# Performance work log

Measured on AMD Instinct MI355X. Metric: run time of the kernel, lower is better.

Reference implementation:

```python
import jax, jax.numpy as jnp
import numpy as np

B, C, IMG, P, D, L, NH, DFF = 8, 2, 256, 16, 1024, 8, 16, 4096
HP = IMG // P          # 16 patches per side
N = HP * HP            # 256 patch tokens
S = N + 1              # + cls token
HD = D // NH           # 64 head dim


def _ln(x, w, b, eps=1e-5):
    mu = x.mean(-1, keepdims=True)
    var = ((x - mu) ** 2).mean(-1, keepdims=True)
    return (x - mu) * jax.lax.rsqrt(var + eps) * w + b


def _decay_mask():
    # RetNetRelPos2d(D, NH, initial_value=1, heads_range=NH): per-head log-decay
    decay = jnp.log(1.0 - 2.0 ** (-1.0 - NH * jnp.arange(NH, dtype=jnp.float32) / NH))
    idx = jnp.arange(HP)
    gy, gx = jnp.meshgrid(idx, idx, indexing='ij')
    grid = jnp.stack([gy.ravel(), gx.ravel()], -1)                 # [N,2]
    dist = jnp.abs(grid[:, None] - grid[None, :]).sum(-1)          # [N,N] Manhattan
    mask = decay[:, None, None] * dist.astype(jnp.float32)        # [NH,N,N]
    return jnp.pad(mask, ((0, 0), (1, 0), (1, 0)))                 # cls: zero decay


def setup_inputs() -> dict:
    key = jax.random.key(0)
    ks = iter(jax.random.split(key, 16))
    g = lambda shape: jax.random.normal(next(ks), shape, jnp.float32) * 0.02
    return dict(
        imgs=jax.random.normal(next(ks), (B, C, IMG, IMG), jnp.float32),
        patch_w=g((C, P, P, D)), patch_b=jnp.zeros((D,), jnp.float32),
        cls_tok=g((1, 1, D)),
        ln1_w=jnp.ones((L, D), jnp.float32), ln1_b=jnp.zeros((L, D), jnp.float32),
        wq=g((L, D, D)), wk=g((L, D, D)), wv=g((L, D, D)),
        bq=jnp.zeros((L, D), jnp.float32), bk=jnp.zeros((L, D), jnp.float32), bv=jnp.zeros((L, D), jnp.float32),
        wo=g((L, D, D)), bo=jnp.zeros((L, D), jnp.float32),
        ln2_w=jnp.ones((L, D), jnp.float32), ln2_b=jnp.zeros((L, D), jnp.float32),
        w1=g((L, D, DFF)), b1=jnp.zeros((L, DFF), jnp.float32),
        w2=g((L, DFF, D)), b2=jnp.zeros((L, D), jnp.float32),
        normf_w=jnp.ones((D,), jnp.float32), normf_b=jnp.zeros((D,), jnp.float32),
        enpred_w=g((D, P * P * 2)), enpred_b=jnp.zeros((P * P * 2,), jnp.float32),
    )


def reference(imgs, patch_w, patch_b, cls_tok, ln1_w, ln1_b, wq, wk, wv, bq, bk, bv,
              wo, bo, ln2_w, ln2_b, w1, b1, w2, b2, normf_w, normf_b, enpred_w, enpred_b):
    b = imgs.shape[0]
    # PatchEmbed: conv with stride==kernel == patch extraction + linear
    xp = imgs.reshape(b, C, HP, P, HP, P)
    x = jnp.einsum('nchpwq,cpqd->nhwd', xp, patch_w).reshape(b, N, D) + patch_b
    residual = x
    x = jnp.concatenate([jnp.broadcast_to(cls_tok, (b, 1, D)), x], axis=1)  # [b,S,D]
    mask = _decay_mask()  # [NH,S,S]
    scale = HD ** -0.5
    for i in range(L):  # RMT blocks: pre-LN MaSA (softmax(qk*scale + decay)) + pre-LN GELU MLP
        h = _ln(x, ln1_w[i], ln1_b[i])
        q = (h @ wq[i] + bq[i]).reshape(b, S, NH, HD)
        k = (h @ wk[i] + bk[i]).reshape(b, S, NH, HD)
        v = (h @ wv[i] + bv[i]).reshape(b, S, NH, HD)
        logits = jnp.einsum('bqhd,bkhd->bhqk', q, k) * scale + mask
        attn = jax.nn.softmax(logits, axis=-1)
        o = jnp.einsum('bhqk,bkhd->bqhd', attn, v).reshape(b, S, D)
        x = x + o @ wo[i] + bo[i]
        h = _ln(x, ln2_w[i], ln2_b[i])
        x = x + jax.nn.gelu(h @ w1[i] + b1[i], approximate=False) @ w2[i] + b2[i]
    x = _ln(x, normf_w, normf_b)
    # PGSA on patch tokens as [b,D,HP,HP]
    t = x[:, 1:, :].transpose(0, 2, 1).reshape(b, D, HP, HP)
    n = HP * HP - 1
    mu = t.mean(axis=(2, 3), keepdims=True)
    xm2 = (t - mu) ** 2
    y = xm2 / (4.0 * (xm2.sum(axis=(2, 3), keepdims=True) / n + 1e-4)) + 0.5
    t = t * jax.nn.sigmoid(y)
    tokens = t.reshape(b, D, N).transpose(0, 2, 1) + residual
    pred = tokens @ enpred_w + enpred_b  # [b,N,P*P*2]
    # unpatchify -> [b,2,IMG,IMG]
    u = pred.reshape(b, HP, HP, P, P, 2)
    return jnp.einsum('nhwpqc->nchpwq', u).reshape(b, 2, IMG, IMG)
```

## Files before the change

### kernel.cpp

```cpp
#include <hip/hip_runtime.h>
#include <cstdint>
#include <cstddef>

#define BB    8
#define CCH   2
#define IMGD  256
#define PDIM  16
#define DD    1024
#define LLAY  8
#define NHEAD 16
#define DFFD  4096
#define NTOK  256
#define SD    257
#define HDD   64
#define MTOK  (BB*SD)
#define MPAT  (BB*NTOK)
#define MPAD  2176
#define KPAD  288

typedef unsigned short u16;
typedef __bf16 bf16x8 __attribute__((ext_vector_type(8)));
typedef float  f32x4  __attribute__((ext_vector_type(4)));

__device__ __forceinline__ u16 f2bf(float f) {
    uint32_t u = __float_as_uint(f);
    u += 0x7FFF + ((u >> 16) & 1);
    return (u16)(u >> 16);
}
__device__ __forceinline__ int imin(int a, int b) { return a < b ? a : b; }

#define GLB(p)  ((const __attribute__((address_space(1))) void*)(uintptr_t)(p))
#define LDSP(p) ((__attribute__((address_space(3))) void*)(uint32_t)(uintptr_t)(p))

__device__ __forceinline__ void tp64(const float* __restrict__ W,
                                     u16* __restrict__ WT, int K, int N,
                                     int k0, int n0, float (*t)[65])
{
    const int c = threadIdx.x & 63, r4 = threadIdx.x >> 6;
    #pragma unroll
    for (int i = 0; i < 16; ++i) {
        const int r = i * 4 + r4;
        t[r][c] = W[(size_t)(k0 + r) * N + n0 + c];
    }
    __syncthreads();
    #pragma unroll
    for (int i = 0; i < 16; ++i) {
        const int r = i * 4 + r4;
        WT[(size_t)(n0 + r) * K + k0 + c] = f2bf(t[c][r]);
    }
}

__device__ __forceinline__ void tp_dispatch(
    int t, const float* wqN, const float* wkN, const float* wvN,
    const float* woN, const float* w1N, const float* w2N,
    u16* WTqkvN, u16* WTwoN, u16* WTw1N, u16* WTw2N, float (*tb)[65])
{
    if (t < 768) {
        const int which = t >> 8, local = t & 255;
        const float* W = which == 0 ? wqN : which == 1 ? wkN : wvN;
        tp64(W, WTqkvN + (size_t)which * 1024 * DD, DD, DD,
             (local >> 4) * 64, (local & 15) * 64, tb);
    } else if (t < 1024) {
        const int local = t - 768;
        tp64(woN, WTwoN, DD, DD, (local >> 4) * 64, (local & 15) * 64, tb);
    } else if (t < 2048) {
        const int local = t - 1024;
        tp64(w1N, WTw1N, DD, DFFD, (local >> 6) * 64, (local & 63) * 64, tb);
    } else {
        const int local = t - 2048;
        tp64(w2N, WTw2N, DFFD, DD, (local >> 4) * 64, (local & 15) * 64, tb);
    }
}

__global__ __launch_bounds__(256) void mlp1_tp(
    const u16* __restrict__ A, const u16* __restrict__ BT,
    const float* __restrict__ bias, u16* __restrict__ Cout, int M,
    const float* __restrict__ wqN, const float* __restrict__ wkN,
    const float* __restrict__ wvN, const float* __restrict__ woN,
    const float* __restrict__ w1N, const float* __restrict__ w2N,
    u16* __restrict__ WTqkvN, u16* __restrict__ WTwoN,
    u16* __restrict__ WTw1N, u16* __restrict__ WTw2N)
{
    __shared__ float smem[64 * 65];
    if (blockIdx.y >= 17) {
        const int t = (blockIdx.y - 17) * 32 + blockIdx.x;
        tp_dispatch(t, wqN, wkN, wvN, woN, w1N, w2N,
                    WTqkvN, WTwoN, WTw1N, WTw2N, (float(*)[65])smem);
        return;
    }
    u16* lds = (u16*)smem;
    const int N = DFFD, K = DD;
    const int tid = threadIdx.x, wid = tid >> 6, lane = tid & 63;
    const int m0 = blockIdx.y * 128, n0 = blockIdx.x * 128;
    const int wm = (wid >> 1) * 64, wn = (wid & 1) * 64;
    const int srow = lane >> 2, scol = (lane & 3) * 8;
    const int l15 = lane & 15, loct = lane >> 4;

    f32x4 acc[4][4] = {};
    const size_t arow = (size_t)(m0 + wid * 16 + srow) * K + scol;
    const size_t brow = (size_t)(n0 + wid * 16 + srow) * K + scol;
    u16* ldsA = lds + wid * 512;
    u16* ldsB = lds + 4096 + wid * 512;

    for (int k0 = 0; k0 < K; k0 += 32) {
        __builtin_amdgcn_global_load_lds(GLB(A  + arow + k0),                 LDSP(ldsA),        16, 0, 0);
        __builtin_amdgcn_global_load_lds(GLB(A  + arow + (size_t)64*K + k0),  LDSP(ldsA + 2048), 16, 0, 0);
        __builtin_amdgcn_global_load_lds(GLB(BT + brow + k0),                 LDSP(ldsB),        16, 0, 0);
        __builtin_amdgcn_global_load_lds(GLB(BT + brow + (size_t)64*K + k0),  LDSP(ldsB + 2048), 16, 0, 0);
        __syncthreads();
        bf16x8 af[4], bfr[4];
        #pragma unroll
        for (int i = 0; i < 4; ++i)
            af[i] = *(const bf16x8*)(lds + (wm + i * 16 + l15) * 32 + loct * 8);
        #pragma unroll
        for (int j = 0; j < 4; ++j)
            bfr[j] = *(const bf16x8*)(lds + 4096 + (wn + j * 16 + l15) * 32 + loct * 8);
        #pragma unroll
        for (int i = 0; i < 4; ++i)
            #pragma unroll
            for (int j = 0; j < 4; ++j)
                acc[i][j] = __builtin_amdgcn_mfma_f32_16x16x32_bf16(af[i], bfr[j], acc[i][j], 0, 0, 0);
        __syncthreads();
    }

    #pragma unroll
    for (int j = 0; j < 4; ++j) {
        const int col = n0 + wn + j * 16 + l15;
        const float bv = bias[col];
        #pragma unroll
        for (int i = 0; i < 4; ++i) {
            const int rbase = m0 + wm + i * 16 + loct * 4;
            #pragma unroll
            for (int r = 0; r < 4; ++r) {
                const int row = rbase + r;
                if (row < M) {
                    float v = acc[i][j][r] + bv;
                    v = 0.5f * v * (1.f + erff(v * 0.70710678118654752f));
                    Cout[(size_t)row * N + col] = f2bf(v);
                }
            }
        }
    }
}

__global__ __launch_bounds__(256) void patch_tp(
    const u16* __restrict__ A, const u16* __restrict__ BT,
    const float* __restrict__ bias, float* __restrict__ Cout,
    const float* __restrict__ wq0, const float* __restrict__ wk0,
    const float* __restrict__ wv0, const float* __restrict__ wo0,
    const float* __restrict__ w10, const float* __restrict__ w20,
    u16* __restrict__ WTqkv0, u16* __restrict__ WTwo0,
    u16* __restrict__ WTw10, u16* __restrict__ WTw20)
{
    __shared__ float smem[64 * 65];
    if (blockIdx.y >= 32) {
        const int t = (blockIdx.y - 32) * 16 + blockIdx.x;
        tp_dispatch(t, wq0, wk0, wv0, wo0, w10, w20,
                    WTqkv0, WTwo0, WTw10, WTw20, (float(*)[65])smem);
        return;
    }
    u16* lds = (u16*)smem;
    const int N = DD, K = 512;
    const int tid = threadIdx.x, wid = tid >> 6, lane = tid & 63;
    const int m0 = blockIdx.y * 64, n0 = blockIdx.x * 64;
    const int wm = (wid >> 1) * 32, wn = (wid & 1) * 32;
    const int srow = lane >> 2, scol = (lane & 3) * 8;
    const int l15 = lane & 15, loct = lane >> 4;

    f32x4 acc[2][2] = {};
    const size_t arow = (size_t)(m0 + wid * 16 + srow) * K + scol;
    const size_t brow = (size_t)(n0 + wid * 16 + srow) * K + scol;
    u16* ldsA = lds + wid * 512;
    u16* ldsB = lds + 4096 + wid * 512;

    for (int k0 = 0; k0 < K; k0 += 64) {
        __builtin_amdgcn_global_load_lds(GLB(A  + arow + k0),      LDSP(ldsA),        16, 0, 0);
        __builtin_amdgcn_global_load_lds(GLB(A  + arow + k0 + 32), LDSP(ldsA + 2048), 16, 0, 0);
        __builtin_amdgcn_global_load_lds(GLB(BT + brow + k0),      LDSP(ldsB),        16, 0, 0);
        __builtin_amdgcn_global_load_lds(GLB(BT + brow + k0 + 32), LDSP(ldsB + 2048), 16, 0, 0);
        __syncthreads();
        #pragma unroll
        for (int t = 0; t < 2; ++t) {
            bf16x8 af[2], bfr[2];
            #pragma unroll
            for (int i = 0; i < 2; ++i)
                af[i] = *(const bf16x8*)(lds + t * 2048 + (wm + i * 16 + l15) * 32 + loct * 8);
            #pragma unroll
            for (int j = 0; j < 2; ++j)
                bfr[j] = *(const bf16x8*)(lds + 4096 + t * 2048 + (wn + j * 16 + l15) * 32 + loct * 8);
            #pragma unroll
            for (int i = 0; i < 2; ++i)
                #pragma unroll
                for (int j = 0; j < 2; ++j)
                    acc[i][j] = __builtin_amdgcn_mfma_f32_16x16x32_bf16(af[i], bfr[j], acc[i][j], 0, 0, 0);
        }
        __syncthreads();
    }

    #pragma unroll
    for (int j = 0; j < 2; ++j) {
        const int col = n0 + wn + j * 16 + l15;
        const float bv = bias[col];
        #pragma unroll
        for (int i = 0; i < 2; ++i) {
            const int rbase = m0 + wm + i * 16 + loct * 4;
            #pragma unroll
            for (int r = 0; r < 4; ++r) {
                const int row = rbase + r;
                Cout[(size_t)row * N + col] = acc[i][j][r] + bv;
            }
        }
    }
}

__global__ __launch_bounds__(256) void gemm_qkv(
    const u16* __restrict__ A, const u16* __restrict__ BT,
    const float* __restrict__ bq, const float* __restrict__ bk,
    const float* __restrict__ bvp,
    u16* __restrict__ QKb, u16* __restrict__ VTg, int M, int K)
{
    __shared__ u16 lds[8192];
    const int tid = threadIdx.x, wid = tid >> 6, lane = tid & 63;
    const int m0 = blockIdx.y * 128, n0 = blockIdx.x * 128;
    const int wm = (wid >> 1) * 64, wn = (wid & 1) * 64;
    const int srow = lane >> 2, scol = (lane & 3) * 8;
    const int l15 = lane & 15, loct = lane >> 4;

    f32x4 acc[4][4] = {};
    const size_t arow = (size_t)(m0 + wid * 16 + srow) * K + scol;
    const size_t brow = (size_t)(n0 + wid * 16 + srow) * K + scol;
    u16* ldsA = lds + wid * 512;
    u16* ldsB = lds + 4096 + wid * 512;

    for (int k0 = 0; k0 < K; k0 += 32) {
        __builtin_amdgcn_global_load_lds(GLB(A  + arow + k0),                 LDSP(ldsA),        16, 0, 0);
        __builtin_amdgcn_global_load_lds(GLB(A  + arow + (size_t)64*K + k0),  LDSP(ldsA + 2048), 16, 0, 0);
        __builtin_amdgcn_global_load_lds(GLB(BT + brow + k0),                 LDSP(ldsB),        16, 0, 0);
        __builtin_amdgcn_global_load_lds(GLB(BT + brow + (size_t)64*K + k0),  LDSP(ldsB + 2048), 16, 0, 0);
        __syncthreads();
        bf16x8 af[4], bfr[4];
        #pragma unroll
        for (int i = 0; i < 4; ++i)
            af[i] = *(const bf16x8*)(lds + (wm + i * 16 + l15) * 32 + loct * 8);
        #pragma unroll
        for (int j = 0; j < 4; ++j)
            bfr[j] = *(const bf16x8*)(lds + 4096 + (wn + j * 16 + l15) * 32 + loct * 8);
        #pragma unroll
        for (int i = 0; i < 4; ++i)
            #pragma unroll
            for (int j = 0; j < 4; ++j)
                acc[i][j] = __builtin_amdgcn_mfma_f32_16x16x32_bf16(af[i], bfr[j], acc[i][j], 0, 0, 0);
        __syncthreads();
    }

    #pragma unroll
    for (int j = 0; j < 4; ++j) {
        const int col = n0 + wn + j * 16 + l15;
        const float bval = (col < 1024) ? bq[col]
                         : (col < 2048) ? bk[col - 1024]
                                        : bvp[col - 2048];
        #pragma unroll
        for (int i = 0; i < 4; ++i) {
            const int rbase = m0 + wm + i * 16 + loct * 4;
            #pragma unroll
            for (int r = 0; r < 4; ++r) {
                const int row = rbase + r;
                if (row < M) {
                    const float v = acc[i][j][r] + bval;
                    if (col < 2048) {
                        QKb[(size_t)row * 2048 + col] = f2bf(v);
                    } else {
                        const int b = row / SD;
                        const int key = row - b * SD;
                        VTg[((size_t)b * 1024 + (col - 2048)) * KPAD + key] = f2bf(v);
                    }
                }
            }
        }
    }
}

template<int ACT, int OBF>
__global__ __launch_bounds__(256) void gemm64(
    const u16* __restrict__ A, const u16* __restrict__ BT,
    const float* __restrict__ bias, const float* __restrict__ Cin,
    void* __restrict__ Cout, int M, int N, int K)
{
    __shared__ u16 lds[8192];
    const int tid = threadIdx.x, wid = tid >> 6, lane = tid & 63;
    const int m0 = blockIdx.y * 64, n0 = blockIdx.x * 64;
    const int wm = (wid >> 1) * 32, wn = (wid & 1) * 32;
    const int srow = lane >> 2, scol = (lane & 3) * 8;
    const int l15 = lane & 15, loct = lane >> 4;

    f32x4 acc[2][2] = {};
    const size_t arow = (size_t)(m0 + wid * 16 + srow) * K + scol;
    const size_t brow = (size_t)(n0 + wid * 16 + srow) * K + scol;
    u16* ldsA = lds + wid * 512;
    u16* ldsB = lds + 4096 + wid * 512;

    for (int k0 = 0; k0 < K; k0 += 64) {
        __builtin_amdgcn_global_load_lds(GLB(A  + arow + k0),      LDSP(ldsA),        16, 0, 0);
        __builtin_amdgcn_global_load_lds(GLB(A  + arow + k0 + 32), LDSP(ldsA + 2048), 16, 0, 0);
        __builtin_amdgcn_global_load_lds(GLB(BT + brow + k0),      LDSP(ldsB),        16, 0, 0);
        __builtin_amdgcn_global_load_lds(GLB(BT + brow + k0 + 32), LDSP(ldsB + 2048), 16, 0, 0);
        __syncthreads();
        #pragma unroll
        for (int t = 0; t < 2; ++t) {
            bf16x8 af[2], bfr[2];
            #pragma unroll
            for (int i = 0; i < 2; ++i)
                af[i] = *(const bf16x8*)(lds + t * 2048 + (wm + i * 16 + l15) * 32 + loct * 8);
            #pragma unroll
            for (int j = 0; j < 2; ++j)
                bfr[j] = *(const bf16x8*)(lds + 4096 + t * 2048 + (wn + j * 16 + l15) * 32 + loct * 8);
            #pragma unroll
            for (int i = 0; i < 2; ++i)
                #pragma unroll
                for (int j = 0; j < 2; ++j)
                    acc[i][j] = __builtin_amdgcn_mfma_f32_16x16x32_bf16(af[i], bfr[j], acc[i][j], 0, 0, 0);
        }
        __syncthreads();
    }

    #pragma unroll
    for (int j = 0; j < 2; ++j) {
        const int col = n0 + wn + j * 16 + l15;
        const float bv = bias[col];
        #pragma unroll
        for (int i = 0; i < 2; ++i) {
            const int rbase = m0 + wm + i * 16 + loct * 4;
            #pragma unroll
            for (int r = 0; r < 4; ++r) {
                const int row = rbase + r;
                if (row < M) {
                    float v = acc[i][j][r] + bv;
                    if (ACT) v = 0.5f * v * (1.f + erff(v * 0.70710678118654752f));
                    if (Cin) v += Cin[(size_t)row * N + col];
                    if (OBF) ((u16*)Cout)[(size_t)row * N + col] = f2bf(v);
                    else     ((float*)Cout)[(size_t)row * N + col] = v;
                }
            }
        }
    }
}

__global__ __launch_bounds__(256) void attn_fused(
    const u16* __restrict__ QKb, const u16* __restrict__ VTg,
    u16* __restrict__ O)
{
    __shared__ u16 P[4][16][296];
    const int tid = threadIdx.x, wid = tid >> 6, lane = tid & 63;
    const int l15 = lane & 15, loct = lane >> 4;
    const int bh = blockIdx.x, b = bh >> 4, h = bh & 15;
    const int q0 = blockIdx.y * 64 + wid * 16;

    const size_t qkbase = (size_t)b * SD * 2048 + h * 64;
    const u16* qp = QKb + qkbase + (size_t)imin(q0 + l15, SD - 1) * 2048;
    const bf16x8 qf0 = *(const bf16x8*)(qp + loct * 8);
    const bf16x8 qf1 = *(const bf16x8*)(qp + 32 + loct * 8);

    f32x4 s[17];
    #pragma unroll
    for (int nt = 0; nt < 17; ++nt) {
        const u16* kp = QKb + qkbase + (size_t)imin(nt * 16 + l15, SD - 1) * 2048 + 1024;
        const bf16x8 kf0 = *(const bf16x8*)(kp + loct * 8);
        const bf16x8 kf1 = *(const bf16x8*)(kp + 32 + loct * 8);
        f32x4 a = {};
        a = __builtin_amdgcn_mfma_f32_16x16x32_bf16(qf0, kf0, a, 0, 0, 0);
        a = __builtin_amdgcn_mfma_f32_16x16x32_bf16(qf1, kf1, a, 0, 0, 0);
        s[nt] = a;
    }

    const float dec = logf(1.f - exp2f(-1.f - (float)h));
    const int qb = q0 + loct * 4;
    float rmax[4] = {-3.4e38f, -3.4e38f, -3.4e38f, -3.4e38f};
    #pragma unroll
    for (int nt = 0; nt < 17; ++nt) {
        const int key = nt * 16 + l15;
        #pragma unroll
        for (int r = 0; r < 4; ++r) {
            float v;
            if (key >= SD) {
                v = -1e30f;
            } else {
                v = s[nt][r] * 0.125f;
                const int q = qb + r;
                if (q > 0 && key > 0) {
                    const int nq = q - 1, nk = key - 1;
                    const int dist = abs((nq >> 4) - (nk >> 4)) + abs((nq & 15) - (nk & 15));
                    v += dec * (float)dist;
                }
            }
            s[nt][r] = v;
            rmax[r] = fmaxf(rmax[r], v);
        }
    }
    #pragma unroll
    for (int r = 0; r < 4; ++r) {
        #pragma unroll
        for (int m = 1; m < 16; m <<= 1) rmax[r] = fmaxf(rmax[r], __shfl_xor(rmax[r], m));
    }
    float rsum[4] = {0.f, 0.f, 0.f, 0.f};
    #pragma unroll
    for (int nt = 0; nt < 17; ++nt)
        #pragma unroll
        for (int r = 0; r < 4; ++r) {
            const float e = __expf(s[nt][r] - rmax[r]);
            s[nt][r] = e;
            rsum[r] += e;
        }
    #pragma unroll
    for (int r = 0; r < 4; ++r) {
        #pragma unroll
        for (int m = 1; m < 16; m <<= 1) rsum[r] += __shfl_xor(rsum[r], m);
        rsum[r] = 1.f / rsum[r];
    }
    #pragma unroll
    for (int nt = 0; nt < 17; ++nt)
        #pragma unroll
        for (int r = 0; r < 4; ++r)
            P[wid][loct * 4 + r][nt * 16 + l15] = f2bf(s[nt][r] * rsum[r]);
    {
        const int rr = lane >> 2, cc = (lane & 3) * 4;
        #pragma unroll
        for (int i = 0; i < 4; ++i) P[wid][rr][272 + cc + i] = 0;
    }

    f32x4 o[4] = {};
    const u16* vrow = VTg + ((size_t)b * 1024 + h * 64) * KPAD;
    #pragma unroll
    for (int ks = 0; ks < 9; ++ks) {
        const bf16x8 pf = *(const bf16x8*)&P[wid][l15][ks * 32 + loct * 8];
        #pragma unroll
        for (int j = 0; j < 4; ++j) {
            const bf16x8 vf = *(const bf16x8*)(vrow + (size_t)(j * 16 + l15) * KPAD + ks * 32 + loct * 8);
            o[j] = __builtin_amdgcn_mfma_f32_16x16x32_bf16(pf, vf, o[j], 0, 0, 0);
        }
    }
    #pragma unroll
    for (int j = 0; j < 4; ++j)
        #pragma unroll
        for (int r = 0; r < 4; ++r) {
            const int q = qb + r;
            if (q < SD) O[((size_t)(b * SD + q)) * DD + h * 64 + j * 16 + l15] = f2bf(o[j][r]);
        }
}

__global__ __launch_bounds__(256) void transpose_bf16_b(
    const float* __restrict__ W, u16* __restrict__ WT, int K, int N,
    size_t sstrideZ, size_t dstrideZ)
{
    __shared__ float t[64][65];
    tp64(W + (size_t)blockIdx.z * sstrideZ, WT + (size_t)blockIdx.z * dstrideZ,
         K, N, blockIdx.y * 64, blockIdx.x * 64, t);
}

__global__ __launch_bounds__(256) void im2col_k(const float* __restrict__ imgs,
                                                u16* __restrict__ Ao)
{
    const int idx = blockIdx.x * 256 + threadIdx.x;
    const int k = idx & 511, m = idx >> 9;
    const int b = m >> 8, n = m & 255;
    const int hp = n >> 4, wp = n & 15;
    const int c = k >> 8, p = (k >> 4) & 15, q = k & 15;
    Ao[idx] = f2bf(imgs[(((size_t)b * CCH + c) * IMGD + hp * PDIM + p) * IMGD + wp * PDIM + q]);
}

__global__ __launch_bounds__(256) void build_x_k(const float* __restrict__ RES,
                                                 const float* __restrict__ cls,
                                                 float* __restrict__ X)
{
    const int idx = blockIdx.x * 256 + threadIdx.x;
    const int d = idx & 1023;
    const int r = idx >> 10;
    const int b = r / SD;
    const int s = r - b * SD;
    X[idx] = (s == 0) ? cls[d] : RES[((size_t)(b * NTOK + s - 1)) * DD + d];
}

template<int OBF>
__global__ __launch_bounds__(256) void ln_rows(const float* __restrict__ X,
                                               const float* __restrict__ w,
                                               const float* __restrict__ bsrc,
                                               void* __restrict__ Y)
{
    const int wid = threadIdx.x >> 6, lane = threadIdx.x & 63;
    const int row = blockIdx.x * 4 + wid;
    const float* xr = X + (size_t)row * DD;
    float4 v[4];
    float s = 0.f, s2 = 0.f;
    #pragma unroll
    for (int i = 0; i < 4; ++i) {
        v[i] = *(const float4*)(xr + (i * 64 + lane) * 4);
        s  += v[i].x + v[i].y + v[i].z + v[i].w;
        s2 += v[i].x * v[i].x + v[i].y * v[i].y + v[i].z * v[i].z + v[i].w * v[i].w;
    }
    #pragma unroll
    for (int off = 1; off < 64; off <<= 1) {
        s  += __shfl_xor(s, off);
        s2 += __shfl_xor(s2, off);
    }
    const float mu  = s * (1.f / 1024.f);
    const float var = fmaf(-mu, mu, s2 * (1.f / 1024.f));
    const float ri  = rsqrtf(var + 1e-5f);
    #pragma unroll
    for (int i = 0; i < 4; ++i) {
        const float4 wv = *(const float4*)(w + (i * 64 + lane) * 4);
        const float4 bv = *(const float4*)(bsrc + (i * 64 + lane) * 4);
        float4 o;
        o.x = (v[i].x - mu) * ri * wv.x + bv.x;
        o.y = (v[i].y - mu) * ri * wv.y + bv.y;
        o.z = (v[i].z - mu) * ri * wv.z + bv.z;
        o.w = (v[i].w - mu) * ri * wv.w + bv.w;
        if (OBF) {
            ushort4 o4 = make_ushort4(f2bf(o.x), f2bf(o.y), f2bf(o.z), f2bf(o.w));
            *(ushort4*)((u16*)Y + (size_t)row * DD + (i * 64 + lane) * 4) = o4;
        } else {
            *(float4*)((float*)Y + (size_t)row * DD + (i * 64 + lane) * 4) = o;
        }
    }
}

__global__ __launch_bounds__(256) void pgsa_k(const float* __restrict__ Xf,
                                              const float* __restrict__ RES,
                                              u16* __restrict__ TOK)
{
    const int bd = blockIdx.x;
    const int b = bd >> 10, dch = bd & 1023;
    const int n = threadIdx.x;
    const float t = Xf[((size_t)(b * SD + 1 + n)) * DD + dch];
    __shared__ float red[4];
    float s = t;
    #pragma unroll
    for (int off = 1; off < 64; off <<= 1) s += __shfl_xor(s, off);
    if ((n & 63) == 0) red[n >> 6] = s;
    __syncthreads();
    const float mu = (red[0] + red[1] + red[2] + red[3]) * (1.f / 256.f);
    const float xm = t - mu;
    const float xm2 = xm * xm;
    __syncthreads();
    float s2 = xm2;
    #pragma unroll
    for (int off = 1; off < 64; off <<= 1) s2 += __shfl_xor(s2, off);
    if ((n & 63) == 0) red[n >> 6] = s2;
    __syncthreads();
    const float tot2 = red[0] + red[1] + red[2] + red[3];
    const float y = xm2 / (4.f * (tot2 * (1.f / 255.f) + 1e-4f)) + 0.5f;
    const float sig = 1.f / (1.f + expf(-y));
    const size_t ri = ((size_t)b * NTOK + n) * DD + dch;
    TOK[ri] = f2bf(fmaf(t, sig, RES[ri]));
}

__global__ __launch_bounds__(256) void unpatch_k(const float* __restrict__ PRED,
                                                 float* __restrict__ out)
{
    const int idx = blockIdx.x * 256 + threadIdx.x;
    const int j = idx & 255, i = (idx >> 8) & 255;
    const int c = (idx >> 16) & 1, b = idx >> 17;
    const int hp = i >> 4, p = i & 15, wp = j >> 4, q = j & 15;
    out[idx] = PRED[((size_t)b * NTOK + hp * 16 + wp) * 512 + (p * 16 + q) * 2 + c];
}

extern "C" void kernel_launch(void* const* d_in, const int* in_sizes, int n_in,
                              void* d_out, int out_size, void* d_ws, size_t ws_size,
                              hipStream_t stream)
{
    const float* imgs     = (const float*)d_in[0];
    const float* patch_w  = (const float*)d_in[1];
    const float* patch_b  = (const float*)d_in[2];
    const float* cls_tok  = (const float*)d_in[3];
    const float* ln1_w    = (const float*)d_in[4];
    const float* ln1_b    = (const float*)d_in[5];
    const float* wq       = (const float*)d_in[6];
    const float* wk       = (const float*)d_in[7];
    const float* wv       = (const float*)d_in[8];
    const float* bq       = (const float*)d_in[9];
    const float* bk       = (const float*)d_in[10];
    const float* bv       = (const float*)d_in[11];
    const float* wo       = (const float*)d_in[12];
    const float* bo       = (const float*)d_in[13];
    const float* ln2_w    = (const float*)d_in[14];
    const float* ln2_b    = (const float*)d_in[15];
    const float* w1       = (const float*)d_in[16];
    const float* b1       = (const float*)d_in[17];
    const float* w2       = (const float*)d_in[18];
    const float* b2       = (const float*)d_in[19];
    const float* normf_w  = (const float*)d_in[20];
    const float* normf_b  = (const float*)d_in[21];
    const float* enpred_w = (const float*)d_in[22];
    const float* enpred_b = (const float*)d_in[23];
    float* out = (float*)d_out;

    char* w = (char*)d_ws;
    float* X     = (float*)w;            w += (size_t)MTOK * DD * 4;
    float* RES   = (float*)w;            w += (size_t)MPAT * DD * 4;
    u16*   QKb   = (u16*)w;              w += (size_t)MPAD * 2048 * 2;
    u16*   VTg   = (u16*)w;              w += (size_t)BB * 1024 * KPAD * 2;
    char*  UNION = w;                    w += (size_t)MPAD * DFFD * 2;
    u16*   Hb    = (u16*)w;              w += (size_t)MPAD * DD * 2;
    u16*   Ob    = (u16*)w;              w += (size_t)MPAD * DD * 2;
    u16*   WTqkv = (u16*)w;              w += (size_t)LLAY * 3072 * DD * 2;
    u16*   WTwo  = (u16*)w;              w += (size_t)LLAY * DD * DD * 2;
    u16*   WTw1  = (u16*)w;              w += (size_t)LLAY * DFFD * DD * 2;
    u16*   WTw2  = (u16*)w;              w += (size_t)LLAY * DD * DFFD * 2;
    u16*   WTpe  = (u16*)w;              w += (size_t)DD * 512 * 2;
    u16*   WTen  = (u16*)w;              w += (size_t)512 * DD * 2;

    u16*   IM2b  = (u16*)UNION;
    u16*   GELUb = (u16*)UNION;
    float* PRED  = (float*)UNION;
    float* Hf    = (float*)QKb;
    u16*   TOKb  = Hb;

    hipMemsetAsync(VTg, 0, (size_t)BB * 1024 * KPAD * 2, stream);

    hipLaunchKernelGGL(transpose_bf16_b, dim3(DD / 64, 512 / 64, 1), dim3(256), 0, stream,
                       patch_w, WTpe, 512, DD, (size_t)0, (size_t)0);
    hipLaunchKernelGGL(transpose_bf16_b, dim3(512 / 64, DD / 64, 1), dim3(256), 0, stream,
                       enpred_w, WTen, DD, 512, (size_t)0, (size_t)0);
    hipLaunchKernelGGL(im2col_k, dim3(4096), dim3(256), 0, stream, imgs, IM2b);

    hipLaunchKernelGGL(patch_tp, dim3(DD / 64, 32 + 192), dim3(256), 0, stream,
                       IM2b, WTpe, patch_b, RES,
                       wq, wk, wv, wo, w1, w2,
                       WTqkv, WTwo, WTw1, WTw2);
    hipLaunchKernelGGL(build_x_k, dim3(MTOK * DD / 256), dim3(256), 0, stream, RES, cls_tok, X);

    for (int i = 0; i < LLAY; ++i) {
        hipLaunchKernelGGL((ln_rows<1>), dim3(MTOK / 4), dim3(256), 0, stream,
                           X, ln1_w + i * DD, ln1_b + i * DD, (void*)Hb);
        hipLaunchKernelGGL(gemm_qkv, dim3(3072 / 128, 17), dim3(256), 0, stream,
                           Hb, WTqkv + (size_t)i * 3072 * DD,
                           bq + i * DD, bk + i * DD, bv + i * DD, QKb, VTg, MTOK, DD);
        hipLaunchKernelGGL(attn_fused, dim3(BB * NHEAD, 5), dim3(256), 0, stream,
                           QKb, VTg, Ob);
        hipLaunchKernelGGL((gemm64<0,0>), dim3(DD / 64, 33), dim3(256), 0, stream,
                           Ob, WTwo + (size_t)i * DD * DD, bo + i * DD, X, (void*)X, MTOK, DD, DD);
        hipLaunchKernelGGL((ln_rows<1>), dim3(MTOK / 4), dim3(256), 0, stream,
                           X, ln2_w + i * DD, ln2_b + i * DD, (void*)Hb);
        if (i < LLAY - 1) {
            const size_t n1 = (size_t)(i + 1);
            hipLaunchKernelGGL(mlp1_tp, dim3(DFFD / 128, 17 + 96), dim3(256), 0, stream,
                               Hb, WTw1 + (size_t)i * DFFD * DD, b1 + i * DFFD, GELUb, MTOK,
                               wq + n1 * DD * DD, wk + n1 * DD * DD, wv + n1 * DD * DD,
                               wo + n1 * DD * DD, w1 + n1 * DD * DFFD, w2 + n1 * DFFD * DD,
                               WTqkv + n1 * 3072 * DD, WTwo + n1 * DD * DD,
                               WTw1 + n1 * DFFD * DD, WTw2 + n1 * DD * DFFD);
        } else {
            hipLaunchKernelGGL(mlp1_tp, dim3(DFFD / 128, 17), dim3(256), 0, stream,
                               Hb, WTw1 + (size_t)i * DFFD * DD, b1 + i * DFFD, GELUb, MTOK,
                               (const float*)nullptr, (const float*)nullptr, (const float*)nullptr,
                               (const float*)nullptr, (const float*)nullptr, (const float*)nullptr,
                               (u16*)nullptr, (u16*)nullptr, (u16*)nullptr, (u16*)nullptr);
        }
        hipLaunchKernelGGL((gemm64<0,0>), dim3(DD / 64, 33), dim3(256), 0, stream,
                           GELUb, WTw2 + (size_t)i * DD * DFFD, b2 + i * DD, X, (void*)X, MTOK, DD, DFFD);
    }

    hipLaunchKernelGGL((ln_rows<0>), dim3(MTOK / 4), dim3(256), 0, stream, X, normf_w, normf_b, (void*)Hf);
    hipLaunchKernelGGL(pgsa_k, dim3(BB * DD), dim3(256), 0, stream, Hf, RES, TOKb);
    hipLaunchKernelGGL((gemm64<0,0>), dim3(512 / 64, MPAT / 64), dim3(256), 0, stream,
                       TOKb, WTen, enpred_b, (const float*)nullptr, (void*)PRED, MPAT, 512, DD);
    hipLaunchKernelGGL(unpatch_k, dim3(4096), dim3(256), 0, stream, PRED, out);
}
```

Before: 1.942 ms.

## Split-K the MLP down-projection and fold partial reduction into next LayerNorm

Replaces the 64x64-tile down-projection GEMM (K=4096) with a 128x128-tile split-K=4 kernel that writes fp32 partials, which the following LayerNorm kernel sums together with the bias and residual before normalising. QKV GEMM now writes V into a unified QKV buffer with coalesced stores, and a separate tiled transpose kernel builds the V^T layout, replacing the scattered strided stores. This is meant to raise parallelism on the long-K GEMM and remove uncoalesced writes, at the cost of extra fp32 partial traffic and one more launch per layer.

```diff
diff --git a/kernel.cpp b/kernel.cpp
--- a/kernel.cpp
+++ b/kernel.cpp
@@ -17,6 +17,7 @@
 #define MPAT  (BB*NTOK)
 #define MPAD  2176
 #define KPAD  288
+#define QSTR  3072
 
 typedef unsigned short u16;
 typedef __bf16 bf16x8 __attribute__((ext_vector_type(8)));
@@ -143,6 +144,145 @@
     }
 }
 
+template<int SPLIT>
+__global__ __launch_bounds__(256) void gemm128_skp(
+    const u16* __restrict__ A, const u16* __restrict__ BT,
+    float* __restrict__ P, int M, int N, int K)
+{
+    __shared__ u16 lds[8192];
+    const int tid = threadIdx.x, wid = tid >> 6, lane = tid & 63;
+    const int m0 = blockIdx.y * 128, n0 = blockIdx.x * 128;
+    const int wm = (wid >> 1) * 64, wn = (wid & 1) * 64;
+    const int srow = lane >> 2, scol = (lane & 3) * 8;
+    const int l15 = lane & 15, loct = lane >> 4;
+    const int Ks = K / SPLIT;
+    const int kb = blockIdx.z * Ks;
+
+    f32x4 acc[4][4] = {};
+    const size_t arow = (size_t)(m0 + wid * 16 + srow) * K + scol + kb;
+    const size_t brow = (size_t)(n0 + wid * 16 + srow) * K + scol + kb;
+    u16* ldsA = lds + wid * 512;
+    u16* ldsB = lds + 4096 + wid * 512;
+
+    for (int k0 = 0; k0 < Ks; k0 += 32) {
+        __builtin_amdgcn_global_load_lds(GLB(A  + arow + k0),                 LDSP(ldsA),        16, 0, 0);
+        __builtin_amdgcn_global_load_lds(GLB(A  + arow + (size_t)64*K + k0),  LDSP(ldsA + 2048), 16, 0, 0);
+        __builtin_amdgcn_global_load_lds(GLB(BT + brow + k0),                 LDSP(ldsB),        16, 0, 0);
+        __builtin_amdgcn_global_load_lds(GLB(BT + brow + (size_t)64*K + k0),  LDSP(ldsB + 2048), 16, 0, 0);
+        __syncthreads();
+        bf16x8 af[4], bfr[4];
+        #pragma unroll
+        for (int i = 0; i < 4; ++i)
+            af[i] = *(const bf16x8*)(lds + (wm + i * 16 + l15) * 32 + loct * 8);
+        #pragma unroll
+        for (int j = 0; j < 4; ++j)
+            bfr[j] = *(const bf16x8*)(lds + 4096 + (wn + j * 16 + l15) * 32 + loct * 8);
+        #pragma unroll
+        for (int i = 0; i < 4; ++i)
+            #pragma unroll
+            for (int j = 0; j < 4; ++j)
+                acc[i][j] = __builtin_amdgcn_mfma_f32_16x16x32_bf16(af[i], bfr[j], acc[i][j], 0, 0, 0);
+        __syncthreads();
+    }
+
+    float* Pz = P + (size_t)blockIdx.z * M * N;
+    #pragma unroll
+    for (int j = 0; j < 4; ++j) {
+        const int col = n0 + wn + j * 16 + l15;
+        #pragma unroll
+        for (int i = 0; i < 4; ++i) {
+            const int rbase = m0 + wm + i * 16 + loct * 4;
+            #pragma unroll
+            for (int r = 0; r < 4; ++r) {
+                const int row = rbase + r;
+                if (row < M) Pz[(size_t)row * N + col] = acc[i][j][r];
+            }
+        }
+    }
+}
+
+__global__ __launch_bounds__(256) void gemm_qkv(
+    const u16* __restrict__ A, const u16* __restrict__ BT,
+    const float* __restrict__ bq, const float* __restrict__ bk,
+    const float* __restrict__ bvp,
+    u16* __restrict__ QKVb, int M, int K)
+{
+    __shared__ u16 lds[8192];
+    const int tid = threadIdx.x, wid = tid >> 6, lane = tid & 63;
+    const int m0 = blockIdx.y * 128, n0 = blockIdx.x * 128;
+    const int wm = (wid >> 1) * 64, wn = (wid & 1) * 64;
+    const int srow = lane >> 2, scol = (lane & 3) * 8;
+    const int l15 = lane & 15, loct = lane >> 4;
+
+    f32x4 acc[4][4] = {};
+    const size_t arow = (size_t)(m0 + wid * 16 + srow) * K + scol;
+    const size_t brow = (size_t)(n0 + wid * 16 + srow) * K + scol;
+    u16* ldsA = lds + wid * 512;
+    u16* ldsB = lds + 4096 + wid * 512;
+
+    for (int k0 = 0; k0 < K; k0 += 32) {
+        __builtin_amdgcn_global_load_lds(GLB(A  + arow + k0),                 LDSP(ldsA),        16, 0, 0);
+        __builtin_amdgcn_global_load_lds(GLB(A  + arow + (size_t)64*K + k0),  LDSP(ldsA + 2048), 16, 0, 0);
+        __builtin_amdgcn_global_load_lds(GLB(BT + brow + k0),                 LDSP(ldsB),        16, 0, 0);
+        __builtin_amdgcn_global_load_lds(GLB(BT + brow + (size_t)64*K + k0),  LDSP(ldsB + 2048), 16, 0, 0);
+        __syncthreads();
+        bf16x8 af[4], bfr[4];
+        #pragma unroll
+        for (int i = 0; i < 4; ++i)
+            af[i] = *(const bf16x8*)(lds + (wm + i * 16 + l15) * 32 + loct * 8);
+        #pragma unroll
+        for (int j = 0; j < 4; ++j)
+            bfr[j] = *(const bf16x8*)(lds + 4096 + (wn + j * 16 + l15) * 32 + loct * 8);
+        #pragma unroll
+        for (int i = 0; i < 4; ++i)
+            #pragma unroll
+            for (int j = 0; j < 4; ++j)
+                acc[i][j] = __builtin_amdgcn_mfma_f32_16x16x32_bf16(af[i], bfr[j], acc[i][j], 0, 0, 0);
+        __syncthreads();
+    }
+
+    #pragma unroll
+    for (int j = 0; j < 4; ++j) {
+        const int col = n0 + wn + j * 16 + l15;
+        const float bval = (col < 1024) ? bq[col]
+                         : (col < 2048) ? bk[col - 1024]
+                                        : bvp[col - 2048];
+        #pragma unroll
+        for (int i = 0; i < 4; ++i) {
+            const int rbase = m0 + wm + i * 16 + loct * 4;
+            #pragma unroll
+            for (int r = 0; r < 4; ++r) {
+                const int row = rbase + r;
+                if (row < M)
+                    QKVb[(size_t)row * QSTR + col] = f2bf(acc[i][j][r] + bval);
+            }
+        }
+    }
+}
+
+__global__ __launch_bounds__(256) void vt_k(const u16* __restrict__ QKVb,
+                                            u16* __restrict__ VTg)
+{
+    __shared__ u16 t[64][66];
+    const int h0 = blockIdx.x * 64, k0 = blockIdx.y * 64, b = blockIdx.z;
+    const int c = threadIdx.x & 63, r4 = threadIdx.x >> 6;
+    #pragma unroll
+    for (int i = 0; i < 16; ++i) {
+        const int key = k0 + i * 4 + r4;
+        t[i * 4 + r4][c] = (key < SD)
+            ? QKVb[((size_t)(b * SD + key)) * QSTR + 2048 + h0 + c] : (u16)0;
+    }
+    __syncthreads();
+    const int key = k0 + c;
+    if (key < KPAD) {
+        #pragma unroll
+        for (int i = 0; i < 16; ++i) {
+            const int hd = i * 4 + r4;
+            VTg[((size_t)(b * 1024 + h0 + hd)) * KPAD + key] = t[c][hd];
+        }
+    }
+}
+
 __global__ __launch_bounds__(256) void patch_tp(
     const u16* __restrict__ A, const u16* __restrict__ BT,
     const float* __restrict__ bias, float* __restrict__ Cout,
@@ -208,73 +348,6 @@
             for (int r = 0; r < 4; ++r) {
                 const int row = rbase + r;
                 Cout[(size_t)row * N + col] = acc[i][j][r] + bv;
-            }
-        }
-    }
-}
-
-__global__ __launch_bounds__(256) void gemm_qkv(
-    const u16* __restrict__ A, const u16* __restrict__ BT,
-    const float* __restrict__ bq, const float* __restrict__ bk,
-    const float* __restrict__ bvp,
-    u16* __restrict__ QKb, u16* __restrict__ VTg, int M, int K)
-{
-    __shared__ u16 lds[8192];
-    const int tid = threadIdx.x, wid = tid >> 6, lane = tid & 63;
-    const int m0 = blockIdx.y * 128, n0 = blockIdx.x * 128;
-    const int wm = (wid >> 1) * 64, wn = (wid & 1) * 64;
-    const int srow = lane >> 2, scol = (lane & 3) * 8;
-    const int l15 = lane & 15, loct = lane >> 4;
-
-    f32x4 acc[4][4] = {};
-    const size_t arow = (size_t)(m0 + wid * 16 + srow) * K + scol;
-    const size_t brow = (size_t)(n0 + wid * 16 + srow) * K + scol;
-    u16* ldsA = lds + wid * 512;
-    u16* ldsB = lds + 4096 + wid * 512;
-
-    for (int k0 = 0; k0 < K; k0 += 32) {
-        __builtin_amdgcn_global_load_lds(GLB(A  + arow + k0),                 LDSP(ldsA),        16, 0, 0);
-        __builtin_amdgcn_global_load_lds(GLB(A  + arow + (size_t)64*K + k0),  LDSP(ldsA + 2048), 16, 0, 0);
-        __builtin_amdgcn_global_load_lds(GLB(BT + brow + k0),                 LDSP(ldsB),        16, 0, 0);
-        __builtin_amdgcn_global_load_lds(GLB(BT + brow + (size_t)64*K + k0),  LDSP(ldsB + 2048), 16, 0, 0);
-        __syncthreads();
-        bf16x8 af[4], bfr[4];
-        #pragma unroll
-        for (int i = 0; i < 4; ++i)
-            af[i] = *(const bf16x8*)(lds + (wm + i * 16 + l15) * 32 + loct * 8);
-        #pragma unroll
-        for (int j = 0; j < 4; ++j)
-            bfr[j] = *(const bf16x8*)(lds + 4096 + (wn + j * 16 + l15) * 32 + loct * 8);
-        #pragma unroll
-        for (int i = 0; i < 4; ++i)
-            #pragma unroll
-            for (int j = 0; j < 4; ++j)
-                acc[i][j] = __builtin_amdgcn_mfma_f32_16x16x32_bf16(af[i], bfr[j], acc[i][j], 0, 0, 0);
-        __syncthreads();
-    }
-
-    #pragma unroll
-    for (int j = 0; j < 4; ++j) {
-        const int col = n0 + wn + j * 16 + l15;
-        const float bval = (col < 1024) ? bq[col]
-                         : (col < 2048) ? bk[col - 1024]
-                                        : bvp[col - 2048];
-        #pragma unroll
-        for (int i = 0; i < 4; ++i) {
-            const int rbase = m0 + wm + i * 16 + loct * 4;
-            #pragma unroll
-            for (int r = 0; r < 4; ++r) {
-                const int row = rbase + r;
-                if (row < M) {
-                    const float v = acc[i][j][r] + bval;
-                    if (col < 2048) {
-                        QKb[(size_t)row * 2048 + col] = f2bf(v);
-                    } else {
-                        const int b = row / SD;
-                        const int key = row - b * SD;
-                        VTg[((size_t)b * 1024 + (col - 2048)) * KPAD + key] = f2bf(v);
-                    }
-                }
             }
         }
     }
@@ -346,7 +419,7 @@
 }
 
 __global__ __launch_bounds__(256) void attn_fused(
-    const u16* __restrict__ QKb, const u16* __restrict__ VTg,
+    const u16* __restrict__ QKVb, const u16* __restrict__ VTg,
     u16* __restrict__ O)
 {
     __shared__ u16 P[4][16][296];
@@ -355,15 +428,15 @@
     const int bh = blockIdx.x, b = bh >> 4, h = bh & 15;
     const int q0 = blockIdx.y * 64 + wid * 16;
 
-    const size_t qkbase = (size_t)b * SD * 2048 + h * 64;
-    const u16* qp = QKb + qkbase + (size_t)imin(q0 + l15, SD - 1) * 2048;
+    const size_t qkbase = (size_t)b * SD * QSTR + h * 64;
+    const u16* qp = QKVb + qkbase + (size_t)imin(q0 + l15, SD - 1) * QSTR;
     const bf16x8 qf0 = *(const bf16x8*)(qp + loct * 8);
     const bf16x8 qf1 = *(const bf16x8*)(qp + 32 + loct * 8);
 
     f32x4 s[17];
     #pragma unroll
     for (int nt = 0; nt < 17; ++nt) {
-        const u16* kp = QKb + qkbase + (size_t)imin(nt * 16 + l15, SD - 1) * 2048 + 1024;
+        const u16* kp = QKVb + qkbase + (size_t)imin(nt * 16 + l15, SD - 1) * QSTR + 1024;
         const bf16x8 kf0 = *(const bf16x8*)(kp + loct * 8);
         const bf16x8 kf1 = *(const bf16x8*)(kp + 32 + loct * 8);
         f32x4 a = {};
@@ -479,20 +552,32 @@
     X[idx] = (s == 0) ? cls[d] : RES[((size_t)(b * NTOK + s - 1)) * DD + d];
 }
 
-template<int OBF>
-__global__ __launch_bounds__(256) void ln_rows(const float* __restrict__ X,
-                                               const float* __restrict__ w,
-                                               const float* __restrict__ bsrc,
-                                               void* __restrict__ Y)
+template<int NP, int OBF>
+__global__ __launch_bounds__(256) void ln_rows_c(
+    float* __restrict__ X, const float* __restrict__ PB, size_t pstride,
+    const float* __restrict__ badd,
+    const float* __restrict__ w, const float* __restrict__ bsrc,
+    void* __restrict__ Y)
 {
     const int wid = threadIdx.x >> 6, lane = threadIdx.x & 63;
     const int row = blockIdx.x * 4 + wid;
-    const float* xr = X + (size_t)row * DD;
+    float* xr = X + (size_t)row * DD;
     float4 v[4];
     float s = 0.f, s2 = 0.f;
     #pragma unroll
     for (int i = 0; i < 4; ++i) {
-        v[i] = *(const float4*)(xr + (i * 64 + lane) * 4);
+        const int cc = (i * 64 + lane) * 4;
+        v[i] = *(const float4*)(xr + cc);
+        if (NP) {
+            const float4 bb = *(const float4*)(badd + cc);
+            v[i].x += bb.x; v[i].y += bb.y; v[i].z += bb.z; v[i].w += bb.w;
+            #pragma unroll
+            for (int p = 0; p < NP; ++p) {
+                const float4 pv = *(const float4*)(PB + (size_t)p * pstride + (size_t)row * DD + cc);
+                v[i].x += pv.x; v[i].y += pv.y; v[i].z += pv.z; v[i].w += pv.w;
+            }
+            *(float4*)(xr + cc) = v[i];
+        }
         s  += v[i].x + v[i].y + v[i].z + v[i].w;
         s2 += v[i].x * v[i].x + v[i].y * v[i].y + v[i].z * v[i].z + v[i].w * v[i].w;
     }
@@ -506,8 +591,9 @@
     const float ri  = rsqrtf(var + 1e-5f);
     #pragma unroll
     for (int i = 0; i < 4; ++i) {
-        const float4 wv = *(const float4*)(w + (i * 64 + lane) * 4);
-        const float4 bv = *(const float4*)(bsrc + (i * 64 + lane) * 4);
+        const int cc = (i * 64 + lane) * 4;
+        const float4 wv = *(const float4*)(w + cc);
+        const float4 bv = *(const float4*)(bsrc + cc);
         float4 o;
         o.x = (v[i].x - mu) * ri * wv.x + bv.x;
         o.y = (v[i].y - mu) * ri * wv.y + bv.y;
@@ -515,9 +601,9 @@
         o.w = (v[i].w - mu) * ri * wv.w + bv.w;
         if (OBF) {
             ushort4 o4 = make_ushort4(f2bf(o.x), f2bf(o.y), f2bf(o.z), f2bf(o.w));
-            *(ushort4*)((u16*)Y + (size_t)row * DD + (i * 64 + lane) * 4) = o4;
+            *(ushort4*)((u16*)Y + (size_t)row * DD + cc) = o4;
         } else {
-            *(float4*)((float*)Y + (size_t)row * DD + (i * 64 + lane) * 4) = o;
+            *(float4*)((float*)Y + (size_t)row * DD + cc) = o;
         }
     }
 }
@@ -595,11 +681,12 @@
     char* w = (char*)d_ws;
     float* X     = (float*)w;            w += (size_t)MTOK * DD * 4;
     float* RES   = (float*)w;            w += (size_t)MPAT * DD * 4;
-    u16*   QKb   = (u16*)w;              w += (size_t)MPAD * 2048 * 2;
+    u16*   QKVb  = (u16*)w;              w += (size_t)MPAD * QSTR * 2;
     u16*   VTg   = (u16*)w;              w += (size_t)BB * 1024 * KPAD * 2;
     char*  UNION = w;                    w += (size_t)MPAD * DFFD * 2;
     u16*   Hb    = (u16*)w;              w += (size_t)MPAD * DD * 2;
     u16*   Ob    = (u16*)w;              w += (size_t)MPAD * DD * 2;
+    float* PART  = (float*)w;            w += (size_t)4 * MTOK * DD * 4;
     u16*   WTqkv = (u16*)w;              w += (size_t)LLAY * 3072 * DD * 2;
     u16*   WTwo  = (u16*)w;              w += (size_t)LLAY * DD * DD * 2;
     u16*   WTw1  = (u16*)w;              w += (size_t)LLAY * DFFD * DD * 2;
@@ -610,10 +697,9 @@
     u16*   IM2b  = (u16*)UNION;
     u16*   GELUb = (u16*)UNION;
     float* PRED  = (float*)UNION;
-    float* Hf    = (float*)QKb;
+    float* Hf    = (float*)QKVb;
     u16*   TOKb  = Hb;
-
-    hipMemsetAsync(VTg, 0, (size_t)BB * 1024 * KPAD * 2, stream);
+    const size_t PSTR = (size_t)MTOK * DD;
 
     hipLaunchKernelGGL(transpose_bf16_b, dim3(DD / 64, 512 / 64, 1), dim3(256), 0, stream,
                        patch_w, WTpe, 512, DD, (size_t)0, (size_t)0);
@@ -628,17 +714,25 @@
     hipLaunchKernelGGL(build_x_k, dim3(MTOK * DD / 256), dim3(256), 0, stream, RES, cls_tok, X);
 
     for (int i = 0; i < LLAY; ++i) {
-        hipLaunchKernelGGL((ln_rows<1>), dim3(MTOK / 4), dim3(256), 0, stream,
-                           X, ln1_w + i * DD, ln1_b + i * DD, (void*)Hb);
+        if (i == 0)
+            hipLaunchKernelGGL((ln_rows_c<0,1>), dim3(MTOK / 4), dim3(256), 0, stream,
+                               X, (const float*)nullptr, (size_t)0, (const float*)nullptr,
+                               ln1_w + i * DD, ln1_b + i * DD, (void*)Hb);
+        else
+            hipLaunchKernelGGL((ln_rows_c<4,1>), dim3(MTOK / 4), dim3(256), 0, stream,
+                               X, PART, PSTR, b2 + (i - 1) * DD,
+                               ln1_w + i * DD, ln1_b + i * DD, (void*)Hb);
         hipLaunchKernelGGL(gemm_qkv, dim3(3072 / 128, 17), dim3(256), 0, stream,
                            Hb, WTqkv + (size_t)i * 3072 * DD,
-                           bq + i * DD, bk + i * DD, bv + i * DD, QKb, VTg, MTOK, DD);
+                           bq + i * DD, bk + i * DD, bv + i * DD, QKVb, MTOK, DD);
+        hipLaunchKernelGGL(vt_k, dim3(16, 5, BB), dim3(256), 0, stream, QKVb, VTg);
         hipLaunchKernelGGL(attn_fused, dim3(BB * NHEAD, 5), dim3(256), 0, stream,
-                           QKb, VTg, Ob);
+                           QKVb, VTg, Ob);
         hipLaunchKernelGGL((gemm64<0,0>), dim3(DD / 64, 33), dim3(256), 0, stream,
                            Ob, WTwo + (size_t)i * DD * DD, bo + i * DD, X, (void*)X, MTOK, DD, DD);
-        hipLaunchKernelGGL((ln_rows<1>), dim3(MTOK / 4), dim3(256), 0, stream,
-                           X, ln2_w + i * DD, ln2_b + i * DD, (void*)Hb);
+        hipLaunchKernelGGL((ln_rows_c<0,1>), dim3(MTOK / 4), dim3(256), 0, stream,
+                           X, (const float*)nullptr, (size_t)0, (const float*)nullptr,
+                           ln2_w + i * DD, ln2_b + i * DD, (void*)Hb);
         if (i < LLAY - 1) {
             const size_t n1 = (size_t)(i + 1);
             hipLaunchKernelGGL(mlp1_tp, dim3(DFFD / 128, 17 + 96), dim3(256), 0, stream,
@@ -654,11 +748,12 @@
                                (const float*)nullptr, (const float*)nullptr, (const float*)nullptr,
                                (u16*)nullptr, (u16*)nullptr, (u16*)nullptr, (u16*)nullptr);
         }
-        hipLaunchKernelGGL((gemm64<0,0>), dim3(DD / 64, 33), dim3(256), 0, stream,
-                           GELUb, WTw2 + (size_t)i * DD * DFFD, b2 + i * DD, X, (void*)X, MTOK, DD, DFFD);
-    }
-
-    hipLaunchKernelGGL((ln_rows<0>), dim3(MTOK / 4), dim3(256), 0, stream, X, normf_w, normf_b, (void*)Hf);
+        hipLaunchKernelGGL((gemm128_skp<4>), dim3(DD / 128, 17, 4), dim3(256), 0, stream,
+                           GELUb, WTw2 + (size_t)i * DD * DFFD, PART, MTOK, DD, DFFD);
+    }
+
+    hipLaunchKernelGGL((ln_rows_c<4,0>), dim3(MTOK / 4), dim3(256), 0, stream,
+                       X, PART, PSTR, b2 + (LLAY - 1) * DD, normf_w, normf_b, (void*)Hf);
     hipLaunchKernelGGL(pgsa_k, dim3(BB * DD), dim3(256), 0, stream, Hf, RES, TOKb);
     hipLaunchKernelGGL((gemm64<0,0>), dim3(512 / 64, MPAT / 64), dim3(256), 0, stream,
                        TOKb, WTen, enpred_b, (const float*)nullptr, (void*)PRED, MPAT, 512, DD);
```

Measured after the change: 1.925 ms. About the same (-0.9%).
